# Optimization experiments

Hardware: AMD Instinct MI355X
Metric: run time of the kernel (lower is better)

Reference implementation:

```python
import jax, jax.numpy as jnp
import numpy as np

N, H, W, D, K = 32, 36, 36, 512, 64
POOL = 3  # pool_list=[3] -> 3x3 grid of regions
EPS = 1e-12


def setup_inputs() -> dict:
    key = jax.random.key(0)
    k1, k2, k3 = jax.random.split(key, 3)
    x = jax.random.normal(k1, (N, H, W, D), dtype=jnp.float32)
    W_conv = jax.random.normal(k2, (D, K), dtype=jnp.float32) * 0.05
    C = jax.random.normal(k3, (D, K), dtype=jnp.float32) * 0.05
    return {"x": x, "W_conv": W_conv, "C": C}


def _l2norm(v, axis):
    return v / jnp.sqrt(jnp.sum(v * v, axis=axis, keepdims=True) + EPS)


def _encode_vlad(xm, W_conv, C):
    # xm: [N, h, w, D]
    s = jnp.einsum('nhwd,dk->nhwk', xm, W_conv)          # 1x1 conv, no bias
    a = jax.nn.softmax(s, axis=-1)                        # soft assignment [N,h,w,K]
    # Faithful to sum_hw a * (x[...,None] - C) without the [N,h,w,D,K] blow-up:
    # = einsum(x, a) - C * sum_hw(a)
    asum = jnp.sum(a, axis=(1, 2))                        # [N, K]
    v = jnp.einsum('nhwd,nhwk->ndk', xm, a) - C[None] * asum[:, None, :]  # [N, D, K]
    # intra-normalization: normalize each cluster's residual over D
    v = _l2norm(v, axis=1)                                # [N, D, K]
    v = v.reshape(v.shape[0], -1)                         # flatten (row-major, matches tf)
    v = _l2norm(v, axis=-1)                               # [N, D*K]
    return v


def reference(x, W_conv, C):
    n, h, w, d = x.shape
    rl, cl = h / POOL, w / POOL
    outs = []
    for jy in range(POOL):
        for ix in range(POOL):
            y1, y2 = int(round(jy * rl)), int(round(jy * rl + rl))
            x1, x2 = int(round(ix * cl)), int(round(ix * cl + cl))
            outs.append(_encode_vlad(x[:, y1:y2, x1:x2, :], W_conv, C))
    return jnp.concatenate(outs, axis=1)  # [N, POOL*POOL*D*K]
```

## Files before the change

### kernel.cpp

```cpp
#include <hip/hip_runtime.h>

typedef __attribute__((ext_vector_type(4))) float f32x4;
typedef __attribute__((ext_vector_type(8))) short short8;

#define EPSF 1e-12f

__device__ __forceinline__ ushort bf16rne(float x) {
  uint u = __float_as_uint(x);
  u += 0x7fffu + ((u >> 16) & 1u);
  return (ushort)(u >> 16);
}
__device__ __forceinline__ float bf2f(ushort h) {
  return __uint_as_float(((uint)h) << 16);
}
__device__ __forceinline__ void cvt8hl(float4 v0, float4 v1, short8& h8, short8& l8) {
  float vals[8] = {v0.x, v0.y, v0.z, v0.w, v1.x, v1.y, v1.z, v1.w};
#pragma unroll
  for (int j = 0; j < 8; ++j) {
    ushort h = bf16rne(vals[j]);
    h8[j] = (short)h;
    l8[j] = (short)bf16rne(vals[j] - bf2f(h));
  }
}
__device__ __forceinline__ f32x4 mfma16(short8 a, short8 b, f32x4 c) {
  return __builtin_amdgcn_mfma_f32_16x16x32_bf16(a, b, c, 0, 0, 0);
}

__global__ __launch_bounds__(256) void k0_wt(const float* __restrict__ W,
                                             ushort* __restrict__ ws2) {
  int k = blockIdx.x;
  int mi = k >> 4, l15k = k & 15;
  for (int task = threadIdx.x; task < 512; task += 256) {
    int dg8 = task >> 3, j = task & 7;
    int d = dg8 * 8 + j;
    int s2 = dg8 >> 2, hi16d = dg8 & 3;
    int l = hi16d * 16 + l15k;
    float v = W[(size_t)d * 64 + k];
    ushort h = bf16rne(v);
    size_t idx = ((size_t)(s2 * 4 + mi) * 64 + l) * 8 + j;
    ws2[idx] = h;
    ws2[32768 + idx] = bf16rne(v - bf2f(h));
  }
}

__global__ __launch_bounds__(512, 4) void k1_assign(
    const float* __restrict__ x, const ushort* __restrict__ ws2,
    float4* __restrict__ aT_ws, float* __restrict__ asum_ws) {
  __shared__ char sm[26112];
  float4* buf = (float4*)sm;
  ushort* atH = (ushort*)sm;
  ushort* atL = (ushort*)(sm + 7168);
  float* accbuf = (float*)sm;
  float* smax = (float*)(sm + 24576);
  float* ssum = (float*)(sm + 25344);

  int b = blockIdx.x;
  int region = b / 3, third = b % 3;
  int n = region / 9, r = region % 9;
  int y1 = (r / 3) * 12, x1 = (r % 3) * 12;
  int p0 = third * 48;
  int t = threadIdx.x;
  int w = t >> 6;
  int mi = w & 3, ks = w >> 2;
  int lane = t & 63, l15 = lane & 15, hi16 = lane >> 4;
  const float* xn = x + (size_t)n * (36 * 36 * 512);

  const float* srcA;
  const float* srcB = nullptr;
  {
    int G = t;
    int p = G >> 4, sgS = G & 15;
    int dg = (sgS & 8) | ((sgS & 7) ^ (p & 7));
    int pr = p0 + p;
    srcA = xn + ((size_t)(y1 + pr / 12) * 36 + (x1 + pr % 12)) * 512 + dg * 4;
  }
  if (t < 256) {
    int G = 512 + t;
    int p = G >> 4, sgS = G & 15;
    int dg = (sgS & 8) | ((sgS & 7) ^ (p & 7));
    int pr = p0 + p;
    srcB = xn + ((size_t)(y1 + pr / 12) * 36 + (x1 + pr % 12)) * 512 + dg * 4;
  }

  f32x4 acc[3];
#pragma unroll
  for (int ni = 0; ni < 3; ++ni) acc[ni] = (f32x4){0.f, 0.f, 0.f, 0.f};

  float4 ra = *(const float4*)srcA;
  float4 rb = (t < 256) ? *(const float4*)srcB : ra;

  for (int c = 0; c < 8; ++c) {
    __syncthreads();
    float4* bufc = buf + (size_t)(c & 1) * 768;
    bufc[t] = ra;
    if (t < 256) bufc[512 + t] = rb;
    __syncthreads();
    if (c < 7) {
      ra = *(const float4*)(srcA + (c + 1) * 64);
      if (t < 256) rb = *(const float4*)(srcB + (c + 1) * 64);
    }
    const ushort* aPtr = ws2 + ((size_t)((c * 2 + ks) * 4 + mi) * 64 + lane) * 8;
    short8 aH = *(const short8*)aPtr;
    short8 aL = *(const short8*)(aPtr + 32768);
    int dg0 = ks * 8 + hi16 * 2;
#pragma unroll
    for (int ni = 0; ni < 3; ++ni) {
      int p = ni * 16 + l15;
      int sg0 = (dg0 & 8) | ((dg0 & 7) ^ (p & 7));
      float4 lo = bufc[p * 16 + sg0];
      float4 hi = bufc[p * 16 + (sg0 ^ 1)];
      short8 bH, bL;
      cvt8hl(lo, hi, bH, bL);
      f32x4 a0 = acc[ni];
      a0 = mfma16(aH, bH, a0);
      a0 = mfma16(aH, bL, a0);
      a0 = mfma16(aL, bH, a0);
      acc[ni] = a0;
    }
  }
  __syncthreads();

  if (ks == 1) {
    float* dst = accbuf + (mi * 64 + lane) * 13;
#pragma unroll
    for (int ni = 0; ni < 3; ++ni)
#pragma unroll
      for (int rr = 0; rr < 4; ++rr) dst[ni * 4 + rr] = acc[ni][rr];
  }
  __syncthreads();

  float lm[3], e[3][4], ls[3];
  if (ks == 0) {
    const float* src = accbuf + (mi * 64 + lane) * 13;
#pragma unroll
    for (int ni = 0; ni < 3; ++ni)
#pragma unroll
      for (int rr = 0; rr < 4; ++rr) acc[ni][rr] += src[ni * 4 + rr];

#pragma unroll
    for (int ni = 0; ni < 3; ++ni) {
      float m = fmaxf(fmaxf(acc[ni][0], acc[ni][1]), fmaxf(acc[ni][2], acc[ni][3]));
      m = fmaxf(m, __shfl_xor(m, 16));
      m = fmaxf(m, __shfl_xor(m, 32));
      lm[ni] = m;
    }
    if (hi16 == 0)
#pragma unroll
      for (int ni = 0; ni < 3; ++ni) smax[mi * 48 + ni * 16 + l15] = lm[ni];
  }
  __syncthreads();

  if (ks == 0) {
#pragma unroll
    for (int ni = 0; ni < 3; ++ni) {
      int p = ni * 16 + l15;
      float M = fmaxf(fmaxf(smax[0 * 48 + p], smax[1 * 48 + p]),
                      fmaxf(smax[2 * 48 + p], smax[3 * 48 + p]));
      float s = 0.f;
#pragma unroll
      for (int rr = 0; rr < 4; ++rr) {
        e[ni][rr] = __expf(acc[ni][rr] - M);
        s += e[ni][rr];
      }
      s += __shfl_xor(s, 16);
      s += __shfl_xor(s, 32);
      ls[ni] = s;
    }
    if (hi16 == 0)
#pragma unroll
      for (int ni = 0; ni < 3; ++ni) ssum[mi * 48 + ni * 16 + l15] = ls[ni];
  }
  __syncthreads();

  if (ks == 0) {
    float part[4];
#pragma unroll
    for (int rr = 0; rr < 4; ++rr) part[rr] = 0.f;
#pragma unroll
    for (int ni = 0; ni < 3; ++ni) {
      int p = ni * 16 + l15;
      float S = ssum[0 * 48 + p] + ssum[1 * 48 + p] + ssum[2 * 48 + p] + ssum[3 * 48 + p];
      float inv = 1.f / S;
#pragma unroll
      for (int rr = 0; rr < 4; ++rr) {
        float a = e[ni][rr] * inv;
        part[rr] += a;
        int k = mi * 16 + hi16 * 4 + rr;
        ushort h = bf16rne(a);
        atH[k * 56 + p] = h;
        atL[k * 56 + p] = bf16rne(a - bf2f(h));
      }
    }
#pragma unroll
    for (int rr = 0; rr < 4; ++rr) {
      float s = part[rr];
      s += __shfl_xor(s, 1);
      s += __shfl_xor(s, 2);
      s += __shfl_xor(s, 4);
      s += __shfl_xor(s, 8);
      if (l15 == 0) asum_ws[b * 64 + mi * 16 + hi16 * 4 + rr] = s;
    }
  }
  __syncthreads();

  {
    float4* dst = aT_ws + (size_t)region * 2432;
    for (int i = t; i < 768; i += 512) {
      int plane = i / 384;
      int rem = i - plane * 384;
      int row = rem / 6, c4 = rem - row * 6;
      float4 v = *(const float4*)(sm + plane * 7168 + row * 112 + c4 * 16);
      dst[plane * 1216 + row * 19 + third * 6 + c4] = v;
    }
    if (third == 2) {
      float4 z = {0.f, 0.f, 0.f, 0.f};
      for (int i = t; i < 128; i += 512) {
        int plane = i >> 6, row = i & 63;
        dst[plane * 1216 + row * 19 + 18] = z;
      }
    }
  }
}

__global__ __launch_bounds__(512, 8) void k2_vlad(
    const float* __restrict__ x, const float* __restrict__ C,
    const float4* __restrict__ aT_ws, const float* __restrict__ asum_ws,
    float* __restrict__ out, float* __restrict__ colnorm) {
  __shared__ float4 smv[2504];
  char* sm = (char*)smv;
  ushort* atH = (ushort*)sm;
  ushort* atL = (ushort*)(sm + 19456);
  int* poff = (int*)(sm + 38912);
  float* asumS = (float*)(sm + 39552);
  float* cn2 = (float*)(sm + 39808);

  int b = blockIdx.x;
  int reg = b % 288;
  int dc = b / 288;
  int n = reg / 9, r = reg % 9;
  int d0 = dc * 64;
  int y1 = (r / 3) * 12, x1 = (r % 3) * 12;
  int t = threadIdx.x;
  int w = t >> 6, lane = t & 63, l15 = lane & 15, hi16 = lane >> 4;
  const float* xn = x + (size_t)n * (36 * 36 * 512);

  if (t < 160) poff[t] = (t < 144) ? ((y1 + t / 12) * 36 + (x1 + t % 12)) * 512 : 0;
  if (t < 64) {
    asumS[t] = asum_ws[(reg * 3) * 64 + t] + asum_ws[(reg * 3 + 1) * 64 + t] +
               asum_ws[(reg * 3 + 2) * 64 + t];
    cn2[t] = 0.f;
  }
  {
    const float4* src = aT_ws + (size_t)reg * 2432;
    for (int i = t; i < 2432; i += 512) smv[i] = src[i];
  }
  __syncthreads();

  int mi = w & 3, kh = w >> 2;
  int drow = d0 + mi * 16 + l15;
  const float* xcol = xn + drow;

  f32x4 acc[2];
  acc[0] = (f32x4){0.f, 0.f, 0.f, 0.f};
  acc[1] = (f32x4){0.f, 0.f, 0.f, 0.f};

#pragma unroll
  for (int ks = 0; ks < 5; ++ks) {
    int pb = ks * 32 + hi16 * 8;
    int4 poA = *reinterpret_cast<const int4*>(&poff[pb]);
    int4 poB = *reinterpret_cast<const int4*>(&poff[pb + 4]);
    float av[8];
    av[0] = xcol[poA.x]; av[1] = xcol[poA.y];
    av[2] = xcol[poA.z]; av[3] = xcol[poA.w];
    av[4] = xcol[poB.x]; av[5] = xcol[poB.y];
    av[6] = xcol[poB.z]; av[7] = xcol[poB.w];
    bool valid = (ks < 4) || (hi16 < 2);
    short8 ah, al;
#pragma unroll
    for (int j = 0; j < 8; ++j) {
      float v = valid ? av[j] : 0.f;
      ushort h = bf16rne(v);
      ah[j] = (short)h;
      al[j] = (short)bf16rne(v - bf2f(h));
    }
#pragma unroll
    for (int ni = 0; ni < 2; ++ni) {
      int row = kh * 32 + ni * 16 + l15;
      short8 bh = *(const short8*)(atH + row * 152 + pb);
      short8 bl = *(const short8*)(atL + row * 152 + pb);
      f32x4 a0 = acc[ni];
      a0 = mfma16(ah, bh, a0);
      a0 = mfma16(ah, bl, a0);
      a0 = mfma16(al, bh, a0);
      acc[ni] = a0;
    }
  }

  size_t obase = (size_t)reg * (512 * 64);
#pragma unroll
  for (int ni = 0; ni < 2; ++ni) {
    int k = kh * 32 + ni * 16 + l15;
    float ak = asumS[k];
    float s2 = 0.f;
#pragma unroll
    for (int rr = 0; rr < 4; ++rr) {
      int d = d0 + mi * 16 + hi16 * 4 + rr;
      float v = acc[ni][rr] - C[(size_t)d * 64 + k] * ak;
      out[obase + (size_t)d * 64 + k] = v;
      s2 += v * v;
    }
    atomicAdd(&cn2[k], s2);
  }
  __syncthreads();
  if (t < 64) colnorm[(size_t)(reg * 8 + dc) * 64 + t] = cn2[t];
}

__global__ __launch_bounds__(256) void k3_scale(float* __restrict__ out,
                                                const float* __restrict__ colnorm) {
  int b = blockIdx.x;
  int reg = b % 288;
  int dc = b / 288;

  __shared__ float ratio[64];
  __shared__ float fs[64];
  int t = threadIdx.x;
  float c = 0.f;
  if (t < 64) {
#pragma unroll
    for (int j = 0; j < 8; ++j) c += colnorm[(size_t)(reg * 8 + j) * 64 + t];
    ratio[t] = c / (c + EPSF);
  }
  __syncthreads();
  if (t < 64) {
    float g = 0.f;
#pragma unroll
    for (int j = 0; j < 64; ++j) g += ratio[j];
    fs[t] = rsqrtf(c + EPSF) * rsqrtf(g + EPSF);
  }
  __syncthreads();

  size_t base4 = (((size_t)reg * 512) + (size_t)dc * 128) * 64 / 4;
  float4* o4 = reinterpret_cast<float4*>(out);
  for (int j = 0; j < 8; ++j) {
    size_t idx = base4 + t + 256 * j;
    float4 v = o4[idx];
    int k0 = (int)((idx * 4) & 63);
    v.x *= fs[k0]; v.y *= fs[k0 + 1]; v.z *= fs[k0 + 2]; v.w *= fs[k0 + 3];
    o4[idx] = v;
  }
}

extern "C" void kernel_launch(void* const* d_in, const int* in_sizes, int n_in,
                              void* d_out, int out_size, void* d_ws, size_t ws_size,
                              hipStream_t stream) {
  const float* x = (const float*)d_in[0];
  const float* Wc = (const float*)d_in[1];
  const float* C = (const float*)d_in[2];
  float* out = (float*)d_out;

  char* ws = (char*)d_ws;
  ushort* ws2 = (ushort*)(ws);
  float* asum_ws = (float*)(ws + 131072);
  float* colnorm = (float*)(ws + 352256);
  float4* aT_ws = (float4*)(ws + 942080);

  k0_wt<<<64, 256, 0, stream>>>(Wc, ws2);
  k1_assign<<<864, 512, 0, stream>>>(x, ws2, aT_ws, asum_ws);
  k2_vlad<<<2304, 512, 0, stream>>>(x, C, aT_ws, asum_ws, out, colnorm);
  k3_scale<<<1152, 256, 0, stream>>>(out, colnorm);
}
```

Measured before the change: 88.50 us.

## Restructure assignment kernel into smaller blocks reading x directly without LDS staging

```diff
diff --git a/kernel.cpp b/kernel.cpp
--- a/kernel.cpp
+++ b/kernel.cpp
@@ -43,181 +43,100 @@
   }
 }
 
-__global__ __launch_bounds__(512, 4) void k1_assign(
+__global__ __launch_bounds__(256, 8) void k1_assign(
     const float* __restrict__ x, const ushort* __restrict__ ws2,
     float4* __restrict__ aT_ws, float* __restrict__ asum_ws) {
-  __shared__ char sm[26112];
-  float4* buf = (float4*)sm;
+  __shared__ char sm[4608];
   ushort* atH = (ushort*)sm;
-  ushort* atL = (ushort*)(sm + 7168);
-  float* accbuf = (float*)sm;
-  float* smax = (float*)(sm + 24576);
-  float* ssum = (float*)(sm + 25344);
+  ushort* atL = (ushort*)(sm + 2048);
+  float* smax = (float*)(sm + 4096);
+  float* ssum = (float*)(sm + 4352);
 
   int b = blockIdx.x;
-  int region = b / 3, third = b % 3;
+  int region = b / 9, pc = b % 9;
   int n = region / 9, r = region % 9;
   int y1 = (r / 3) * 12, x1 = (r % 3) * 12;
-  int p0 = third * 48;
   int t = threadIdx.x;
   int w = t >> 6;
-  int mi = w & 3, ks = w >> 2;
   int lane = t & 63, l15 = lane & 15, hi16 = lane >> 4;
   const float* xn = x + (size_t)n * (36 * 36 * 512);
 
-  const float* srcA;
-  const float* srcB = nullptr;
-  {
-    int G = t;
-    int p = G >> 4, sgS = G & 15;
-    int dg = (sgS & 8) | ((sgS & 7) ^ (p & 7));
-    int pr = p0 + p;
-    srcA = xn + ((size_t)(y1 + pr / 12) * 36 + (x1 + pr % 12)) * 512 + dg * 4;
-  }
-  if (t < 256) {
-    int G = 512 + t;
-    int p = G >> 4, sgS = G & 15;
-    int dg = (sgS & 8) | ((sgS & 7) ^ (p & 7));
-    int pr = p0 + p;
-    srcB = xn + ((size_t)(y1 + pr / 12) * 36 + (x1 + pr % 12)) * 512 + dg * 4;
-  }
-
-  f32x4 acc[3];
-#pragma unroll
-  for (int ni = 0; ni < 3; ++ni) acc[ni] = (f32x4){0.f, 0.f, 0.f, 0.f};
-
-  float4 ra = *(const float4*)srcA;
-  float4 rb = (t < 256) ? *(const float4*)srcB : ra;
-
-  for (int c = 0; c < 8; ++c) {
-    __syncthreads();
-    float4* bufc = buf + (size_t)(c & 1) * 768;
-    bufc[t] = ra;
-    if (t < 256) bufc[512 + t] = rb;
-    __syncthreads();
-    if (c < 7) {
-      ra = *(const float4*)(srcA + (c + 1) * 64);
-      if (t < 256) rb = *(const float4*)(srcB + (c + 1) * 64);
-    }
-    const ushort* aPtr = ws2 + ((size_t)((c * 2 + ks) * 4 + mi) * 64 + lane) * 8;
+  int p = pc * 16 + l15;
+  const float* xrow =
+      xn + ((size_t)(y1 + p / 12) * 36 + (x1 + p % 12)) * 512 + hi16 * 8;
+  const ushort* aBase = ws2 + ((size_t)w * 64 + lane) * 8;
+
+  f32x4 acc = (f32x4){0.f, 0.f, 0.f, 0.f};
+
+#pragma unroll
+  for (int s = 0; s < 16; ++s) {
+    const ushort* aPtr = aBase + (size_t)s * 2048;
     short8 aH = *(const short8*)aPtr;
     short8 aL = *(const short8*)(aPtr + 32768);
-    int dg0 = ks * 8 + hi16 * 2;
-#pragma unroll
-    for (int ni = 0; ni < 3; ++ni) {
-      int p = ni * 16 + l15;
-      int sg0 = (dg0 & 8) | ((dg0 & 7) ^ (p & 7));
-      float4 lo = bufc[p * 16 + sg0];
-      float4 hi = bufc[p * 16 + (sg0 ^ 1)];
-      short8 bH, bL;
-      cvt8hl(lo, hi, bH, bL);
-      f32x4 a0 = acc[ni];
-      a0 = mfma16(aH, bH, a0);
-      a0 = mfma16(aH, bL, a0);
-      a0 = mfma16(aL, bH, a0);
-      acc[ni] = a0;
-    }
-  }
-  __syncthreads();
-
-  if (ks == 1) {
-    float* dst = accbuf + (mi * 64 + lane) * 13;
-#pragma unroll
-    for (int ni = 0; ni < 3; ++ni)
-#pragma unroll
-      for (int rr = 0; rr < 4; ++rr) dst[ni * 4 + rr] = acc[ni][rr];
-  }
-  __syncthreads();
-
-  float lm[3], e[3][4], ls[3];
-  if (ks == 0) {
-    const float* src = accbuf + (mi * 64 + lane) * 13;
-#pragma unroll
-    for (int ni = 0; ni < 3; ++ni)
-#pragma unroll
-      for (int rr = 0; rr < 4; ++rr) acc[ni][rr] += src[ni * 4 + rr];
-
-#pragma unroll
-    for (int ni = 0; ni < 3; ++ni) {
-      float m = fmaxf(fmaxf(acc[ni][0], acc[ni][1]), fmaxf(acc[ni][2], acc[ni][3]));
-      m = fmaxf(m, __shfl_xor(m, 16));
-      m = fmaxf(m, __shfl_xor(m, 32));
-      lm[ni] = m;
-    }
-    if (hi16 == 0)
-#pragma unroll
-      for (int ni = 0; ni < 3; ++ni) smax[mi * 48 + ni * 16 + l15] = lm[ni];
-  }
-  __syncthreads();
-
-  if (ks == 0) {
-#pragma unroll
-    for (int ni = 0; ni < 3; ++ni) {
-      int p = ni * 16 + l15;
-      float M = fmaxf(fmaxf(smax[0 * 48 + p], smax[1 * 48 + p]),
-                      fmaxf(smax[2 * 48 + p], smax[3 * 48 + p]));
-      float s = 0.f;
-#pragma unroll
-      for (int rr = 0; rr < 4; ++rr) {
-        e[ni][rr] = __expf(acc[ni][rr] - M);
-        s += e[ni][rr];
-      }
-      s += __shfl_xor(s, 16);
-      s += __shfl_xor(s, 32);
-      ls[ni] = s;
-    }
-    if (hi16 == 0)
-#pragma unroll
-      for (int ni = 0; ni < 3; ++ni) ssum[mi * 48 + ni * 16 + l15] = ls[ni];
-  }
-  __syncthreads();
-
-  if (ks == 0) {
-    float part[4];
-#pragma unroll
-    for (int rr = 0; rr < 4; ++rr) part[rr] = 0.f;
-#pragma unroll
-    for (int ni = 0; ni < 3; ++ni) {
-      int p = ni * 16 + l15;
-      float S = ssum[0 * 48 + p] + ssum[1 * 48 + p] + ssum[2 * 48 + p] + ssum[3 * 48 + p];
-      float inv = 1.f / S;
-#pragma unroll
-      for (int rr = 0; rr < 4; ++rr) {
-        float a = e[ni][rr] * inv;
-        part[rr] += a;
-        int k = mi * 16 + hi16 * 4 + rr;
-        ushort h = bf16rne(a);
-        atH[k * 56 + p] = h;
-        atL[k * 56 + p] = bf16rne(a - bf2f(h));
-      }
-    }
+    float4 v0 = *(const float4*)(xrow + s * 32);
+    float4 v1 = *(const float4*)(xrow + s * 32 + 4);
+    short8 bH, bL;
+    cvt8hl(v0, v1, bH, bL);
+    acc = mfma16(aH, bH, acc);
+    acc = mfma16(aH, bL, acc);
+    acc = mfma16(aL, bH, acc);
+  }
+
+  {
+    float m = fmaxf(fmaxf(acc[0], acc[1]), fmaxf(acc[2], acc[3]));
+    m = fmaxf(m, __shfl_xor(m, 16));
+    m = fmaxf(m, __shfl_xor(m, 32));
+    if (hi16 == 0) smax[w * 16 + l15] = m;
+  }
+  __syncthreads();
+
+  float e[4];
+  {
+    float M = fmaxf(fmaxf(smax[0 * 16 + l15], smax[1 * 16 + l15]),
+                    fmaxf(smax[2 * 16 + l15], smax[3 * 16 + l15]));
+    float s = 0.f;
 #pragma unroll
     for (int rr = 0; rr < 4; ++rr) {
-      float s = part[rr];
+      e[rr] = __expf(acc[rr] - M);
+      s += e[rr];
+    }
+    s += __shfl_xor(s, 16);
+    s += __shfl_xor(s, 32);
+    if (hi16 == 0) ssum[w * 16 + l15] = s;
+  }
+  __syncthreads();
+
+  {
+    float S = ssum[0 * 16 + l15] + ssum[1 * 16 + l15] + ssum[2 * 16 + l15] +
+              ssum[3 * 16 + l15];
+    float inv = 1.f / S;
+#pragma unroll
+    for (int rr = 0; rr < 4; ++rr) {
+      float a = e[rr] * inv;
+      int k = w * 16 + hi16 * 4 + rr;
+      ushort h = bf16rne(a);
+      atH[k * 16 + l15] = h;
+      atL[k * 16 + l15] = bf16rne(a - bf2f(h));
+      float s = a;
       s += __shfl_xor(s, 1);
       s += __shfl_xor(s, 2);
       s += __shfl_xor(s, 4);
       s += __shfl_xor(s, 8);
-      if (l15 == 0) asum_ws[b * 64 + mi * 16 + hi16 * 4 + rr] = s;
+      if (l15 == 0) asum_ws[(size_t)b * 64 + k] = s;
     }
   }
   __syncthreads();
 
   {
     float4* dst = aT_ws + (size_t)region * 2432;
-    for (int i = t; i < 768; i += 512) {
-      int plane = i / 384;
-      int rem = i - plane * 384;
-      int row = rem / 6, c4 = rem - row * 6;
-      float4 v = *(const float4*)(sm + plane * 7168 + row * 112 + c4 * 16);
-      dst[plane * 1216 + row * 19 + third * 6 + c4] = v;
-    }
-    if (third == 2) {
+    int plane = t >> 7, rem = t & 127;
+    int row = rem >> 1, g = rem & 1;
+    float4 v = *(const float4*)(sm + plane * 2048 + row * 32 + g * 16);
+    dst[plane * 1216 + row * 19 + pc * 2 + g] = v;
+    if (pc == 8 && t < 128) {
       float4 z = {0.f, 0.f, 0.f, 0.f};
-      for (int i = t; i < 128; i += 512) {
-        int plane = i >> 6, row = i & 63;
-        dst[plane * 1216 + row * 19 + 18] = z;
-      }
+      int pl = t >> 6, rw = t & 63;
+      dst[pl * 1216 + rw * 19 + 18] = z;
     }
   }
 }
@@ -246,8 +165,10 @@
 
   if (t < 160) poff[t] = (t < 144) ? ((y1 + t / 12) * 36 + (x1 + t % 12)) * 512 : 0;
   if (t < 64) {
-    asumS[t] = asum_ws[(reg * 3) * 64 + t] + asum_ws[(reg * 3 + 1) * 64 + t] +
-               asum_ws[(reg * 3 + 2) * 64 + t];
+    float s = 0.f;
+#pragma unroll
+    for (int i = 0; i < 9; ++i) s += asum_ws[(size_t)(reg * 9 + i) * 64 + t];
+    asumS[t] = s;
     cn2[t] = 0.f;
   }
   {
@@ -361,11 +282,11 @@
   char* ws = (char*)d_ws;
   ushort* ws2 = (ushort*)(ws);
   float* asum_ws = (float*)(ws + 131072);
-  float* colnorm = (float*)(ws + 352256);
-  float4* aT_ws = (float4*)(ws + 942080);
+  float* colnorm = (float*)(ws + 794624);
+  float4* aT_ws = (float4*)(ws + 1384448);
 
   k0_wt<<<64, 256, 0, stream>>>(Wc, ws2);
-  k1_assign<<<864, 512, 0, stream>>>(x, ws2, aT_ws, asum_ws);
+  k1_assign<<<2592, 256, 0, stream>>>(x, ws2, aT_ws, asum_ws);
   k2_vlad<<<2304, 512, 0, stream>>>(x, C, aT_ws, asum_ws, out, colnorm);
   k3_scale<<<1152, 256, 0, stream>>>(out, colnorm);
 }
```

Result: slower. 109.0 us (+23.2%).
